# Kernel tuning notes

Measured on AMD Instinct MI355X. Metric: run time of the kernel, lower is better.

## Reference

```python
import jax, jax.numpy as jnp
import numpy as np

NUM_EXPERTS = 8

def setup_inputs() -> dict:
    key = jax.random.key(0)
    k1, k2, k3, k4, k5 = jax.random.split(key, 5)
    T, D, H, O, E, K = 4096, 1024, 2048, 1024, NUM_EXPERTS, 2
    hidden_states = jax.random.normal(k1, (T, D), dtype=jnp.float32)
    top_k_indices = jax.random.randint(k2, (T, K), 0, E, dtype=jnp.int64)
    top_k_weights = jax.random.uniform(k3, (T, K), dtype=jnp.float32)
    gate_up_proj = jax.random.normal(k4, (E, 2 * H, D), dtype=jnp.float32) * 0.02
    down_proj = jax.random.normal(k5, (E, O, H), dtype=jnp.float32) * 0.02
    return {
        "hidden_states": hidden_states,
        "top_k_indices": top_k_indices,
        "top_k_weights": top_k_weights,
        "gate_up_proj": gate_up_proj,
        "down_proj": down_proj,
    }


def _moe(hidden_states, top_k_weights, gate_up_proj, down_proj, top_k_indices):
    # Mathematically identical to the torch per-token-gather loop, expressed as
    # dense all-expert compute + sparse combine (non-selected experts get weight 0).
    T = hidden_states.shape[0]
    E = gate_up_proj.shape[0]
    # [T, E, 2H]
    gate_up = jnp.einsum('td,ehd->teh', hidden_states, gate_up_proj)
    gate, up = jnp.split(gate_up, 2, axis=-1)
    h = jax.nn.silu(gate) * up  # [T, E, H]
    expert_out = jnp.einsum('teh,eoh->teo', h, down_proj)  # [T, E, O]
    # combine weights: scatter top-k routing weights into [T, E]
    combine = jnp.zeros((T, E), dtype=hidden_states.dtype)
    rows = jnp.arange(T)[:, None]
    combine = combine.at[rows, top_k_indices].add(top_k_weights)
    return jnp.einsum('teo,te->to', expert_out, combine)


def reference(hidden_states, top_k_indices, top_k_weights, gate_up_proj, down_proj):
    return _moe(hidden_states, top_k_weights, gate_up_proj, down_proj, top_k_indices)
```

## Files before the change

kernel.cpp:

```cpp
#include <hip/hip_runtime.h>
#include <stdint.h>

#define TOKS 4096
#define DIM  1024
#define HID  2048
#define OUTD 1024
#define NE   8
#define MP   9216
#define NBR  72

typedef __bf16 bf16;
typedef bf16 bf16x8 __attribute__((ext_vector_type(8)));
typedef float f32x4 __attribute__((ext_vector_type(4)));
typedef __attribute__((address_space(1))) void gvoid;
typedef __attribute__((address_space(3))) void lvoid;

#define WGU_OFF  0ull
#define WD_OFF   (WGU_OFF + 67108864ull)
#define XG_OFF   (WD_OFF  + 33554432ull)
#define H_OFF    (XG_OFF  + 18874368ull)
#define TK_OFF   (H_OFF   + 37748736ull)
#define META_OFF (TK_OFF  + 36864ull)
#define T2S_OFF  (META_OFF + 1024ull)

__device__ __forceinline__ unsigned short f2bf(float f) {
  union { float f; unsigned u; } v; v.f = f;
  unsigned r = (v.u + 0x7FFFu + ((v.u >> 16) & 1u)) >> 16;
  return (unsigned short)r;
}
__device__ __forceinline__ unsigned pack2(float a, float b) {
  return (unsigned)f2bf(a) | ((unsigned)f2bf(b) << 16);
}
__device__ __forceinline__ void cp16(const void* g, void* l) {
  __builtin_amdgcn_global_load_lds((gvoid*)(void*)g, (lvoid*)l, 16, 0, 0);
}

__global__ __launch_bounds__(1024) void route_kernel(const int* __restrict__ idx,
                                                     int* __restrict__ table,
                                                     int* __restrict__ slot_token,
                                                     int* __restrict__ tok2slot) {
  __shared__ int cnt[NE], offs[NE], cur[NE];
  const int tid = threadIdx.x, lane = tid & 63;
  for (int i = tid; i < MP; i += 1024) slot_token[i] = -1;
  if (tid < NE) cnt[tid] = 0;
  __syncthreads();
  int myE[8];
#pragma unroll
  for (int c = 0; c < 8; ++c) myE[c] = idx[c * 1024 + tid];
#pragma unroll
  for (int c = 0; c < 8; ++c) {
    int e = myE[c];
#pragma unroll
    for (int ex = 0; ex < NE; ++ex) {
      unsigned long long m = __ballot(e == ex);
      if (lane == 0 && m) atomicAdd(&cnt[ex], __popcll(m));
    }
  }
  __syncthreads();
  if (tid == 0) {
    int cum = 0;
    for (int e = 0; e < NE; ++e) {
      offs[e] = cum; cur[e] = 0;
      int nb = (cnt[e] + 127) >> 7;
      int bb = cum >> 7;
      for (int b = 0; b < nb; ++b) table[bb + b] = e;
      cum += nb << 7;
    }
    for (int b = cum >> 7; b < NBR; ++b) table[b] = -1;
  }
  __syncthreads();
#pragma unroll
  for (int c = 0; c < 8; ++c) {
    int e = myE[c];
    int pos = 0;
#pragma unroll
    for (int ex = 0; ex < NE; ++ex) {
      unsigned long long m = __ballot(e == ex);
      if (e == ex) {
        int rank = __popcll(m & ((1ull << lane) - 1ull));
        int leader = __ffsll(m) - 1;
        int base = 0;
        if (lane == leader) base = atomicAdd(&cur[ex], __popcll(m));
        base = __shfl(base, leader);
        pos = offs[ex] + base + rank;
      }
    }
    slot_token[pos] = (c * 1024 + tid) >> 1;
    tok2slot[c * 1024 + tid] = pos;
  }
}

__global__ void gather_kernel(const float* __restrict__ X, const int* __restrict__ slot_token,
                              uint4* __restrict__ Xg) {
  int gid = blockIdx.x * 256 + threadIdx.x;
  int row = gid >> 7, j = (gid & 127) << 3;
  int t = slot_token[row];
  uint4 o;
  if (t >= 0) {
    const float4* p = (const float4*)(X + (size_t)t * DIM + j);
    float4 a = p[0], b = p[1];
    o.x = pack2(a.x, a.y); o.y = pack2(a.z, a.w);
    o.z = pack2(b.x, b.y); o.w = pack2(b.z, b.w);
  } else {
    o = uint4{0u, 0u, 0u, 0u};
  }
  Xg[gid] = o;
}

__global__ void convert_kernel(const float4* __restrict__ srcGu, uint2* __restrict__ dstGu,
                               const float4* __restrict__ srcD, uint2* __restrict__ dstD) {
  const int n1 = NE * 2 * HID * DIM / 4;
  int i = blockIdx.x * 256 + threadIdx.x;
  float4 v; uint2* dp;
  if (i < n1) { v = srcGu[i]; dp = dstGu + i; }
  else        { v = srcD[i - n1]; dp = dstD + (i - n1); }
  uint2 o; o.x = pack2(v.x, v.y); o.y = pack2(v.z, v.w);
  *dp = o;
}

__global__ void combine_kernel(const float* __restrict__ Obuf, const int* __restrict__ tok2slot,
                               const float* __restrict__ wts, float4* __restrict__ out) {
  int t = blockIdx.x, c = threadIdx.x;
  int s0 = tok2slot[2 * t], s1 = tok2slot[2 * t + 1];
  float w0 = wts[2 * t], w1 = wts[2 * t + 1];
  float4 a = ((const float4*)(Obuf + (size_t)s0 * OUTD))[c];
  float4 b = ((const float4*)(Obuf + (size_t)s1 * OUTD))[c];
  out[(size_t)t * (OUTD / 4) + c] =
      float4{w0 * a.x + w1 * b.x, w0 * a.y + w1 * b.y, w0 * a.z + w1 * b.z, w0 * a.w + w1 * b.w};
}

__global__ __launch_bounds__(256) void gemm1_kernel(
    const unsigned short* __restrict__ Xg,
    const unsigned short* __restrict__ Wgu,
    unsigned short* __restrict__ Hbuf,
    const int* __restrict__ table) {
  int e = table[blockIdx.y];
  if (e < 0) return;
  const int tid = threadIdx.x;
  const int lane = tid & 63, wave = tid >> 6;
  const int wm = wave >> 1, wn = wave & 1;
  const int lr = lane & 15, quad = lane >> 4;

  __shared__ bf16 As[128 * 64];
  __shared__ bf16 Bg[64 * 64];
  __shared__ bf16 Bu[64 * 64];

  const unsigned short* A_base  = Xg  + (size_t)blockIdx.y * 128 * DIM;
  const unsigned short* Wg_base = Wgu + (size_t)e * 2 * HID * DIM + (size_t)(blockIdx.x * 64) * DIM;
  const unsigned short* Wu_base = Wg_base + (size_t)HID * DIM;

  f32x4 accg[4][2] = {}; f32x4 accu[4][2] = {};

  for (int kt = 0; kt < DIM / 64; ++kt) {
    const int kb = kt * 64;
#pragma unroll
    for (int i = 0; i < 4; ++i) {
      int s = i * 256 + tid, row = s >> 3, pc = s & 7, gc = pc ^ (row & 7);
      cp16(A_base + (size_t)row * DIM + kb + gc * 8, (void*)(As + row * 64 + pc * 8));
    }
#pragma unroll
    for (int i = 0; i < 2; ++i) {
      int s = i * 256 + tid, row = s >> 3, pc = s & 7, gc = pc ^ (row & 7);
      cp16(Wg_base + (size_t)row * DIM + kb + gc * 8, (void*)(Bg + row * 64 + pc * 8));
      cp16(Wu_base + (size_t)row * DIM + kb + gc * 8, (void*)(Bu + row * 64 + pc * 8));
    }
    __syncthreads();
#pragma unroll
    for (int ks = 0; ks < 2; ++ks) {
      bf16x8 a[4], bg[2], bu[2];
#pragma unroll
      for (int i = 0; i < 4; ++i) {
        int row = wm * 64 + i * 16 + lr;
        int pc = (ks * 4 + quad) ^ (row & 7);
        a[i] = *(const bf16x8*)(As + row * 64 + pc * 8);
      }
#pragma unroll
      for (int j = 0; j < 2; ++j) {
        int row = wn * 32 + j * 16 + lr;
        int pc = (ks * 4 + quad) ^ (row & 7);
        bg[j] = *(const bf16x8*)(Bg + row * 64 + pc * 8);
        bu[j] = *(const bf16x8*)(Bu + row * 64 + pc * 8);
      }
#pragma unroll
      for (int i = 0; i < 4; ++i)
#pragma unroll
        for (int j = 0; j < 2; ++j) {
          accg[i][j] = __builtin_amdgcn_mfma_f32_16x16x32_bf16(a[i], bg[j], accg[i][j], 0, 0, 0);
          accu[i][j] = __builtin_amdgcn_mfma_f32_16x16x32_bf16(a[i], bu[j], accu[i][j], 0, 0, 0);
        }
    }
    __syncthreads();
  }

  const int rowBase = blockIdx.y * 128 + wm * 64;
  const int colBase = blockIdx.x * 64 + wn * 32;
#pragma unroll
  for (int i = 0; i < 4; ++i)
#pragma unroll
    for (int r = 0; r < 4; ++r) {
      int row = rowBase + i * 16 + quad * 4 + r;
#pragma unroll
      for (int j = 0; j < 2; ++j) {
        float g = accg[i][j][r], u = accu[i][j][r];
        float s = g / (1.0f + __expf(-g));
        Hbuf[(size_t)row * HID + colBase + j * 16 + lr] = f2bf(s * u);
      }
    }
}

__global__ __launch_bounds__(256) void gemm2_kernel(
    const unsigned short* __restrict__ Hbuf,
    const unsigned short* __restrict__ Wd,
    float* __restrict__ Obuf,
    const int* __restrict__ table) {
  int e = table[blockIdx.y];
  if (e < 0) return;
  const int tid = threadIdx.x;
  const int lane = tid & 63, wave = tid >> 6;
  const int wm = wave >> 1, wn = wave & 1;
  const int lr = lane & 15, quad = lane >> 4;

  __shared__ bf16 As[128 * 64];
  __shared__ bf16 Bs[128 * 64];

  const unsigned short* A_base = Hbuf + (size_t)blockIdx.y * 128 * HID;
  const unsigned short* B_base = Wd + (size_t)e * OUTD * HID + (size_t)(blockIdx.x * 128) * HID;

  f32x4 acc[4][4] = {};

  for (int kt = 0; kt < HID / 64; ++kt) {
    const int kb = kt * 64;
#pragma unroll
    for (int i = 0; i < 4; ++i) {
      int s = i * 256 + tid, row = s >> 3, pc = s & 7, gc = pc ^ (row & 7);
      cp16(A_base + (size_t)row * HID + kb + gc * 8, (void*)(As + row * 64 + pc * 8));
      cp16(B_base + (size_t)row * HID + kb + gc * 8, (void*)(Bs + row * 64 + pc * 8));
    }
    __syncthreads();
#pragma unroll
    for (int ks = 0; ks < 2; ++ks) {
      bf16x8 a[4], b[4];
#pragma unroll
      for (int i = 0; i < 4; ++i) {
        int row = wm * 64 + i * 16 + lr;
        int pc = (ks * 4 + quad) ^ (row & 7);
        a[i] = *(const bf16x8*)(As + row * 64 + pc * 8);
      }
#pragma unroll
      for (int j = 0; j < 4; ++j) {
        int row = wn * 64 + j * 16 + lr;
        int pc = (ks * 4 + quad) ^ (row & 7);
        b[j] = *(const bf16x8*)(Bs + row * 64 + pc * 8);
      }
#pragma unroll
      for (int i = 0; i < 4; ++i)
#pragma unroll
        for (int j = 0; j < 4; ++j)
          acc[i][j] = __builtin_amdgcn_mfma_f32_16x16x32_bf16(a[i], b[j], acc[i][j], 0, 0, 0);
    }
    __syncthreads();
  }

  const int rowBase = blockIdx.y * 128 + wm * 64;
  const int colBase = blockIdx.x * 128 + wn * 64;
#pragma unroll
  for (int i = 0; i < 4; ++i)
#pragma unroll
    for (int r = 0; r < 4; ++r) {
      int row = rowBase + i * 16 + quad * 4 + r;
      float* Orow = Obuf + (size_t)row * OUTD + colBase;
#pragma unroll
      for (int j = 0; j < 4; ++j)
        Orow[j * 16 + lr] = acc[i][j][r];
    }
}

extern "C" void kernel_launch(void* const* d_in, const int* in_sizes, int n_in,
                              void* d_out, int out_size, void* d_ws, size_t ws_size,
                              hipStream_t stream) {
  const float* X     = (const float*)d_in[0];
  const int*   idx   = (const int*)d_in[1];
  const float* wts   = (const float*)d_in[2];
  const float* WguF  = (const float*)d_in[3];
  const float* WdF   = (const float*)d_in[4];
  float* out = (float*)d_out;

  char* base = (char*)d_ws;
  unsigned short* Wgu = (unsigned short*)(base + WGU_OFF);
  unsigned short* Wd  = (unsigned short*)(base + WD_OFF);
  unsigned short* Xg  = (unsigned short*)(base + XG_OFF);
  unsigned short* Hb  = (unsigned short*)(base + H_OFF);
  float* Obuf         = (float*)(base + WGU_OFF);
  int*   slot_token = (int*)(base + TK_OFF);
  int*   table      = (int*)(base + META_OFF);
  int*   tok2slot   = (int*)(base + T2S_OFF);

  route_kernel<<<1, 1024, 0, stream>>>(idx, table, slot_token, tok2slot);
  gather_kernel<<<(MP * 128) / 256, 256, 0, stream>>>(X, slot_token, (uint4*)Xg);
  {
    const int nTot = (NE * 2 * HID * DIM + NE * OUTD * HID) / 4;
    convert_kernel<<<nTot / 256, 256, 0, stream>>>((const float4*)WguF, (uint2*)Wgu,
                                                   (const float4*)WdF, (uint2*)Wd);
  }
  gemm1_kernel<<<dim3(HID / 64, NBR), 256, 0, stream>>>(Xg, Wgu, Hb, table);
  gemm2_kernel<<<dim3(OUTD / 128, NBR), 256, 0, stream>>>(Hb, Wd, Obuf, table);
  combine_kernel<<<TOKS, 256, 0, stream>>>(Obuf, tok2slot, wts, (float4*)out);
}
```

Measured before the change: 438.6 us.

## Switch GEMMs to 32x32 MFMA, enlarge gemm1 tile, split-K gemm2, fuse prep kernels

Merges the gather and weight-conversion kernels into one launch. Both GEMMs move from 16x16x32 to 32x32x16 bf16 MFMA, and gemm1 widens its N tile from 64 to 128 columns for more reuse of the A tile. Gemm2 is split into two K halves that write bf16 partial outputs, and the combine kernel sums them. Launch bounds ask for two blocks per CU. In exchange, gemm1 uses more LDS, and rounding the partial outputs to bf16 adds error.

```diff
diff --git a/kernel.cpp b/kernel.cpp
--- a/kernel.cpp
+++ b/kernel.cpp
@@ -11,7 +11,7 @@
 
 typedef __bf16 bf16;
 typedef bf16 bf16x8 __attribute__((ext_vector_type(8)));
-typedef float f32x4 __attribute__((ext_vector_type(4)));
+typedef float f32x16 __attribute__((ext_vector_type(16)));
 typedef __attribute__((address_space(1))) void gvoid;
 typedef __attribute__((address_space(3))) void lvoid;
 
@@ -22,11 +22,16 @@
 #define TK_OFF   (H_OFF   + 37748736ull)
 #define META_OFF (TK_OFF  + 36864ull)
 #define T2S_OFF  (META_OFF + 1024ull)
+#define O0_OFF   WGU_OFF
+#define O1_OFF   (WGU_OFF + 18874368ull)
 
 __device__ __forceinline__ unsigned short f2bf(float f) {
   union { float f; unsigned u; } v; v.f = f;
   unsigned r = (v.u + 0x7FFFu + ((v.u >> 16) & 1u)) >> 16;
   return (unsigned short)r;
+}
+__device__ __forceinline__ float bf2f(unsigned short h) {
+  union { unsigned u; float f; } v; v.u = ((unsigned)h) << 16; return v.f;
 }
 __device__ __forceinline__ unsigned pack2(float a, float b) {
   return (unsigned)f2bf(a) | ((unsigned)f2bf(b) << 16);
@@ -90,46 +95,38 @@
   }
 }
 
-__global__ void gather_kernel(const float* __restrict__ X, const int* __restrict__ slot_token,
-                              uint4* __restrict__ Xg) {
-  int gid = blockIdx.x * 256 + threadIdx.x;
-  int row = gid >> 7, j = (gid & 127) << 3;
-  int t = slot_token[row];
-  uint4 o;
-  if (t >= 0) {
-    const float4* p = (const float4*)(X + (size_t)t * DIM + j);
-    float4 a = p[0], b = p[1];
-    o.x = pack2(a.x, a.y); o.y = pack2(a.z, a.w);
-    o.z = pack2(b.x, b.y); o.w = pack2(b.z, b.w);
+#define GATHER_B 4608
+__global__ void prep_kernel(const float* __restrict__ X, const int* __restrict__ slot_token,
+                            uint4* __restrict__ Xg,
+                            const float4* __restrict__ srcGu, uint2* __restrict__ dstGu,
+                            const float4* __restrict__ srcD, uint2* __restrict__ dstD) {
+  int bx = blockIdx.x;
+  if (bx < GATHER_B) {
+    int gid = bx * 256 + threadIdx.x;
+    int row = gid >> 7, j = (gid & 127) << 3;
+    int t = slot_token[row];
+    uint4 o;
+    if (t >= 0) {
+      const float4* p = (const float4*)(X + (size_t)t * DIM + j);
+      float4 a = p[0], b = p[1];
+      o.x = pack2(a.x, a.y); o.y = pack2(a.z, a.w);
+      o.z = pack2(b.x, b.y); o.w = pack2(b.z, b.w);
+    } else {
+      o = uint4{0u, 0u, 0u, 0u};
+    }
+    Xg[gid] = o;
   } else {
-    o = uint4{0u, 0u, 0u, 0u};
-  }
-  Xg[gid] = o;
-}
-
-__global__ void convert_kernel(const float4* __restrict__ srcGu, uint2* __restrict__ dstGu,
-                               const float4* __restrict__ srcD, uint2* __restrict__ dstD) {
-  const int n1 = NE * 2 * HID * DIM / 4;
-  int i = blockIdx.x * 256 + threadIdx.x;
-  float4 v; uint2* dp;
-  if (i < n1) { v = srcGu[i]; dp = dstGu + i; }
-  else        { v = srcD[i - n1]; dp = dstD + (i - n1); }
-  uint2 o; o.x = pack2(v.x, v.y); o.y = pack2(v.z, v.w);
-  *dp = o;
-}
-
-__global__ void combine_kernel(const float* __restrict__ Obuf, const int* __restrict__ tok2slot,
-                               const float* __restrict__ wts, float4* __restrict__ out) {
-  int t = blockIdx.x, c = threadIdx.x;
-  int s0 = tok2slot[2 * t], s1 = tok2slot[2 * t + 1];
-  float w0 = wts[2 * t], w1 = wts[2 * t + 1];
-  float4 a = ((const float4*)(Obuf + (size_t)s0 * OUTD))[c];
-  float4 b = ((const float4*)(Obuf + (size_t)s1 * OUTD))[c];
-  out[(size_t)t * (OUTD / 4) + c] =
-      float4{w0 * a.x + w1 * b.x, w0 * a.y + w1 * b.y, w0 * a.z + w1 * b.z, w0 * a.w + w1 * b.w};
-}
-
-__global__ __launch_bounds__(256) void gemm1_kernel(
+    const int n1 = NE * 2 * HID * DIM / 4;
+    int i = (bx - GATHER_B) * 256 + threadIdx.x;
+    float4 v; uint2* dp;
+    if (i < n1) { v = srcGu[i]; dp = dstGu + i; }
+    else        { v = srcD[i - n1]; dp = dstD + (i - n1); }
+    uint2 o; o.x = pack2(v.x, v.y); o.y = pack2(v.z, v.w);
+    *dp = o;
+  }
+}
+
+__global__ __launch_bounds__(256, 2) void gemm1_kernel(
     const unsigned short* __restrict__ Xg,
     const unsigned short* __restrict__ Wgu,
     unsigned short* __restrict__ Hbuf,
@@ -139,140 +136,156 @@
   const int tid = threadIdx.x;
   const int lane = tid & 63, wave = tid >> 6;
   const int wm = wave >> 1, wn = wave & 1;
-  const int lr = lane & 15, quad = lane >> 4;
+  const int l31 = lane & 31, lh = lane >> 5;
 
   __shared__ bf16 As[128 * 64];
-  __shared__ bf16 Bg[64 * 64];
-  __shared__ bf16 Bu[64 * 64];
+  __shared__ bf16 Bg[128 * 64];
+  __shared__ bf16 Bu[128 * 64];
 
   const unsigned short* A_base  = Xg  + (size_t)blockIdx.y * 128 * DIM;
-  const unsigned short* Wg_base = Wgu + (size_t)e * 2 * HID * DIM + (size_t)(blockIdx.x * 64) * DIM;
+  const unsigned short* Wg_base = Wgu + (size_t)e * 2 * HID * DIM + (size_t)(blockIdx.x * 128) * DIM;
   const unsigned short* Wu_base = Wg_base + (size_t)HID * DIM;
 
-  f32x4 accg[4][2] = {}; f32x4 accu[4][2] = {};
+  f32x16 accg[2][2] = {}; f32x16 accu[2][2] = {};
 
   for (int kt = 0; kt < DIM / 64; ++kt) {
     const int kb = kt * 64;
 #pragma unroll
-    for (int i = 0; i < 4; ++i) {
-      int s = i * 256 + tid, row = s >> 3, pc = s & 7, gc = pc ^ (row & 7);
-      cp16(A_base + (size_t)row * DIM + kb + gc * 8, (void*)(As + row * 64 + pc * 8));
-    }
-#pragma unroll
-    for (int i = 0; i < 2; ++i) {
-      int s = i * 256 + tid, row = s >> 3, pc = s & 7, gc = pc ^ (row & 7);
-      cp16(Wg_base + (size_t)row * DIM + kb + gc * 8, (void*)(Bg + row * 64 + pc * 8));
-      cp16(Wu_base + (size_t)row * DIM + kb + gc * 8, (void*)(Bu + row * 64 + pc * 8));
+    for (int i = 0; i < 12; ++i) {
+      int s = i * 256 + tid;
+      int r = (s >> 3) & 127, pc = s & 7, gc = pc ^ (r & 7);
+      const unsigned short* src; bf16* dst;
+      if (i < 4)      { src = A_base;  dst = As; }
+      else if (i < 8) { src = Wg_base; dst = Bg; }
+      else            { src = Wu_base; dst = Bu; }
+      cp16(src + (size_t)r * DIM + kb + gc * 8, (void*)(dst + r * 64 + pc * 8));
     }
     __syncthreads();
 #pragma unroll
-    for (int ks = 0; ks < 2; ++ks) {
-      bf16x8 a[4], bg[2], bu[2];
-#pragma unroll
-      for (int i = 0; i < 4; ++i) {
-        int row = wm * 64 + i * 16 + lr;
-        int pc = (ks * 4 + quad) ^ (row & 7);
-        a[i] = *(const bf16x8*)(As + row * 64 + pc * 8);
-      }
-#pragma unroll
-      for (int j = 0; j < 2; ++j) {
-        int row = wn * 32 + j * 16 + lr;
-        int pc = (ks * 4 + quad) ^ (row & 7);
-        bg[j] = *(const bf16x8*)(Bg + row * 64 + pc * 8);
-        bu[j] = *(const bf16x8*)(Bu + row * 64 + pc * 8);
-      }
-#pragma unroll
-      for (int i = 0; i < 4; ++i)
-#pragma unroll
-        for (int j = 0; j < 2; ++j) {
-          accg[i][j] = __builtin_amdgcn_mfma_f32_16x16x32_bf16(a[i], bg[j], accg[i][j], 0, 0, 0);
-          accu[i][j] = __builtin_amdgcn_mfma_f32_16x16x32_bf16(a[i], bu[j], accu[i][j], 0, 0, 0);
+    for (int ks = 0; ks < 4; ++ks) {
+      const int c = ks * 2 + lh;
+      bf16x8 a[2], bg[2], bu[2];
+#pragma unroll
+      for (int t = 0; t < 2; ++t) {
+        int ar = wm * 64 + t * 32 + l31;
+        a[t]  = *(const bf16x8*)(As + ar * 64 + (c ^ (ar & 7)) * 8);
+        int br = wn * 64 + t * 32 + l31;
+        bg[t] = *(const bf16x8*)(Bg + br * 64 + (c ^ (br & 7)) * 8);
+        bu[t] = *(const bf16x8*)(Bu + br * 64 + (c ^ (br & 7)) * 8);
+      }
+#pragma unroll
+      for (int ti = 0; ti < 2; ++ti)
+#pragma unroll
+        for (int tj = 0; tj < 2; ++tj) {
+          accg[ti][tj] = __builtin_amdgcn_mfma_f32_32x32x16_bf16(a[ti], bg[tj], accg[ti][tj], 0, 0, 0);
+          accu[ti][tj] = __builtin_amdgcn_mfma_f32_32x32x16_bf16(a[ti], bu[tj], accu[ti][tj], 0, 0, 0);
         }
     }
     __syncthreads();
   }
 
   const int rowBase = blockIdx.y * 128 + wm * 64;
-  const int colBase = blockIdx.x * 64 + wn * 32;
-#pragma unroll
-  for (int i = 0; i < 4; ++i)
-#pragma unroll
-    for (int r = 0; r < 4; ++r) {
-      int row = rowBase + i * 16 + quad * 4 + r;
-#pragma unroll
-      for (int j = 0; j < 2; ++j) {
-        float g = accg[i][j][r], u = accu[i][j][r];
+  const int colBase = blockIdx.x * 128 + wn * 64;
+#pragma unroll
+  for (int ti = 0; ti < 2; ++ti)
+#pragma unroll
+    for (int tj = 0; tj < 2; ++tj)
+#pragma unroll
+      for (int r = 0; r < 16; ++r) {
+        int row = rowBase + ti * 32 + (r & 3) + 8 * (r >> 2) + 4 * lh;
+        int col = colBase + tj * 32 + l31;
+        float g = accg[ti][tj][r], u = accu[ti][tj][r];
         float s = g / (1.0f + __expf(-g));
-        Hbuf[(size_t)row * HID + colBase + j * 16 + lr] = f2bf(s * u);
-      }
-    }
-}
-
-__global__ __launch_bounds__(256) void gemm2_kernel(
+        Hbuf[(size_t)row * HID + col] = f2bf(s * u);
+      }
+}
+
+__global__ __launch_bounds__(256, 2) void gemm2_kernel(
     const unsigned short* __restrict__ Hbuf,
     const unsigned short* __restrict__ Wd,
-    float* __restrict__ Obuf,
+    unsigned short* __restrict__ O0,
+    unsigned short* __restrict__ O1,
     const int* __restrict__ table) {
   int e = table[blockIdx.y];
   if (e < 0) return;
   const int tid = threadIdx.x;
   const int lane = tid & 63, wave = tid >> 6;
   const int wm = wave >> 1, wn = wave & 1;
-  const int lr = lane & 15, quad = lane >> 4;
+  const int l31 = lane & 31, lh = lane >> 5;
+  const int kslice = blockIdx.z;
 
   __shared__ bf16 As[128 * 64];
   __shared__ bf16 Bs[128 * 64];
 
-  const unsigned short* A_base = Hbuf + (size_t)blockIdx.y * 128 * HID;
-  const unsigned short* B_base = Wd + (size_t)e * OUTD * HID + (size_t)(blockIdx.x * 128) * HID;
-
-  f32x4 acc[4][4] = {};
-
-  for (int kt = 0; kt < HID / 64; ++kt) {
+  const unsigned short* A_base = Hbuf + (size_t)blockIdx.y * 128 * HID + kslice * (HID / 2);
+  const unsigned short* B_base = Wd + (size_t)e * OUTD * HID + (size_t)(blockIdx.x * 128) * HID
+                               + kslice * (HID / 2);
+
+  f32x16 acc[2][2] = {};
+
+  for (int kt = 0; kt < (HID / 2) / 64; ++kt) {
     const int kb = kt * 64;
 #pragma unroll
-    for (int i = 0; i < 4; ++i) {
-      int s = i * 256 + tid, row = s >> 3, pc = s & 7, gc = pc ^ (row & 7);
-      cp16(A_base + (size_t)row * HID + kb + gc * 8, (void*)(As + row * 64 + pc * 8));
-      cp16(B_base + (size_t)row * HID + kb + gc * 8, (void*)(Bs + row * 64 + pc * 8));
+    for (int i = 0; i < 8; ++i) {
+      int s = i * 256 + tid;
+      int r = (s >> 3) & 127, pc = s & 7, gc = pc ^ (r & 7);
+      const unsigned short* src = (i < 4) ? A_base : B_base;
+      bf16* dst = (i < 4) ? As : Bs;
+      cp16(src + (size_t)r * HID + kb + gc * 8, (void*)(dst + r * 64 + pc * 8));
     }
     __syncthreads();
 #pragma unroll
-    for (int ks = 0; ks < 2; ++ks) {
-      bf16x8 a[4], b[4];
-#pragma unroll
-      for (int i = 0; i < 4; ++i) {
-        int row = wm * 64 + i * 16 + lr;
-        int pc = (ks * 4 + quad) ^ (row & 7);
-        a[i] = *(const bf16x8*)(As + row * 64 + pc * 8);
-      }
-#pragma unroll
-      for (int j = 0; j < 4; ++j) {
-        int row = wn * 64 + j * 16 + lr;
-        int pc = (ks * 4 + quad) ^ (row & 7);
-        b[j] = *(const bf16x8*)(Bs + row * 64 + pc * 8);
-      }
-#pragma unroll
-      for (int i = 0; i < 4; ++i)
-#pragma unroll
-        for (int j = 0; j < 4; ++j)
-          acc[i][j] = __builtin_amdgcn_mfma_f32_16x16x32_bf16(a[i], b[j], acc[i][j], 0, 0, 0);
+    for (int ks = 0; ks < 4; ++ks) {
+      const int c = ks * 2 + lh;
+      bf16x8 a[2], b[2];
+#pragma unroll
+      for (int t = 0; t < 2; ++t) {
+        int ar = wm * 64 + t * 32 + l31;
+        a[t] = *(const bf16x8*)(As + ar * 64 + (c ^ (ar & 7)) * 8);
+        int br = wn * 64 + t * 32 + l31;
+        b[t] = *(const bf16x8*)(Bs + br * 64 + (c ^ (br & 7)) * 8);
+      }
+#pragma unroll
+      for (int ti = 0; ti < 2; ++ti)
+#pragma unroll
+        for (int tj = 0; tj < 2; ++tj)
+          acc[ti][tj] = __builtin_amdgcn_mfma_f32_32x32x16_bf16(a[ti], b[tj], acc[ti][tj], 0, 0, 0);
     }
     __syncthreads();
   }
 
+  unsigned short* O = kslice ? O1 : O0;
   const int rowBase = blockIdx.y * 128 + wm * 64;
   const int colBase = blockIdx.x * 128 + wn * 64;
 #pragma unroll
-  for (int i = 0; i < 4; ++i)
-#pragma unroll
-    for (int r = 0; r < 4; ++r) {
-      int row = rowBase + i * 16 + quad * 4 + r;
-      float* Orow = Obuf + (size_t)row * OUTD + colBase;
-#pragma unroll
-      for (int j = 0; j < 4; ++j)
-        Orow[j * 16 + lr] = acc[i][j][r];
-    }
+  for (int ti = 0; ti < 2; ++ti)
+#pragma unroll
+    for (int tj = 0; tj < 2; ++tj)
+#pragma unroll
+      for (int r = 0; r < 16; ++r) {
+        int row = rowBase + ti * 32 + (r & 3) + 8 * (r >> 2) + 4 * lh;
+        int col = colBase + tj * 32 + l31;
+        O[(size_t)row * OUTD + col] = f2bf(acc[ti][tj][r]);
+      }
+}
+
+__global__ void combine_kernel(const unsigned short* __restrict__ O0,
+                               const unsigned short* __restrict__ O1,
+                               const int* __restrict__ tok2slot,
+                               const float* __restrict__ wts, float4* __restrict__ out) {
+  int t = blockIdx.x, c = threadIdx.x;
+  int s0 = tok2slot[2 * t], s1 = tok2slot[2 * t + 1];
+  float w0 = wts[2 * t], w1 = wts[2 * t + 1];
+  uint2 a0 = ((const uint2*)(O0 + (size_t)s0 * OUTD))[c];
+  uint2 b0 = ((const uint2*)(O1 + (size_t)s0 * OUTD))[c];
+  uint2 a1 = ((const uint2*)(O0 + (size_t)s1 * OUTD))[c];
+  uint2 b1 = ((const uint2*)(O1 + (size_t)s1 * OUTD))[c];
+  float4 o;
+  o.x = w0 * (bf2f(a0.x & 0xFFFF) + bf2f(b0.x & 0xFFFF)) + w1 * (bf2f(a1.x & 0xFFFF) + bf2f(b1.x & 0xFFFF));
+  o.y = w0 * (bf2f(a0.x >> 16)    + bf2f(b0.x >> 16))    + w1 * (bf2f(a1.x >> 16)    + bf2f(b1.x >> 16));
+  o.z = w0 * (bf2f(a0.y & 0xFFFF) + bf2f(b0.y & 0xFFFF)) + w1 * (bf2f(a1.y & 0xFFFF) + bf2f(b1.y & 0xFFFF));
+  o.w = w0 * (bf2f(a0.y >> 16)    + bf2f(b0.y >> 16))    + w1 * (bf2f(a1.y >> 16)    + bf2f(b1.y >> 16));
+  out[(size_t)t * (OUTD / 4) + c] = o;
 }
 
 extern "C" void kernel_launch(void* const* d_in, const int* in_sizes, int n_in,
@@ -290,19 +303,19 @@
   unsigned short* Wd  = (unsigned short*)(base + WD_OFF);
   unsigned short* Xg  = (unsigned short*)(base + XG_OFF);
   unsigned short* Hb  = (unsigned short*)(base + H_OFF);
-  float* Obuf         = (float*)(base + WGU_OFF);
-  int*   slot_token = (int*)(base + TK_OFF);
-  int*   table      = (int*)(base + META_OFF);
-  int*   tok2slot   = (int*)(base + T2S_OFF);
+  unsigned short* O0  = (unsigned short*)(base + O0_OFF);
+  unsigned short* O1  = (unsigned short*)(base + O1_OFF);
+  int* slot_token = (int*)(base + TK_OFF);
+  int* table      = (int*)(base + META_OFF);
+  int* tok2slot   = (int*)(base + T2S_OFF);
 
   route_kernel<<<1, 1024, 0, stream>>>(idx, table, slot_token, tok2slot);
-  gather_kernel<<<(MP * 128) / 256, 256, 0, stream>>>(X, slot_token, (uint4*)Xg);
   {
-    const int nTot = (NE * 2 * HID * DIM + NE * OUTD * HID) / 4;
-    convert_kernel<<<nTot / 256, 256, 0, stream>>>((const float4*)WguF, (uint2*)Wgu,
-                                                   (const float4*)WdF, (uint2*)Wd);
-  }
-  gemm1_kernel<<<dim3(HID / 64, NBR), 256, 0, stream>>>(Xg, Wgu, Hb, table);
-  gemm2_kernel<<<dim3(OUTD / 128, NBR), 256, 0, stream>>>(Hb, Wd, Obuf, table);
-  combine_kernel<<<TOKS, 256, 0, stream>>>(Obuf, tok2slot, wts, (float4*)out);
-}
+    const int convB = (NE * 2 * HID * DIM + NE * OUTD * HID) / 4 / 256;
+    prep_kernel<<<GATHER_B + convB, 256, 0, stream>>>(X, slot_token, (uint4*)Xg,
+        (const float4*)WguF, (uint2*)Wgu, (const float4*)WdF, (uint2*)Wd);
+  }
+  gemm1_kernel<<<dim3(HID / 128, NBR), 256, 0, stream>>>(Xg, Wgu, Hb, table);
+  gemm2_kernel<<<dim3(OUTD / 128, NBR, 2), 256, 0, stream>>>(Hb, Wd, O0, O1, table);
+  combine_kernel<<<TOKS, 256, 0, stream>>>(O0, O1, tok2slot, wts, (float4*)out);
+}
```

Result: no change. 444.5 us (+1.3%).
